# Performance work log

Measured on AMD Instinct MI355X. Metric: run time of the kernel, lower is better.

The kernel has to match this reference:

```python
import jax, jax.numpy as jnp
import numpy as np

D_MODEL = 1024
NUM_HEADS = 16
D_K = D_MODEL // NUM_HEADS  # 64
THETA = 10000.0
BATCH = 2
SEQ = 2048


def _rope_tables(positions, d_k, theta):
    # freq_k = theta**(-2k/d_k), each repeated twice (interleaved layout)
    k = jnp.arange(d_k // 2, dtype=jnp.float32)
    freq = theta ** (-2.0 * k / d_k)            # [d_k/2]
    freq = jnp.repeat(freq, 2)                  # [d_k], pattern f0,f0,f1,f1,...
    ang = positions.astype(jnp.float32)[:, None] * freq[None, :]  # [s, d_k]
    return jnp.cos(ang), jnp.sin(ang)


def _apply_rope(x, cos, sin):
    # x: [b, h, s, d_k]; interleaved rotation: y[0::2]=-x[1::2], y[1::2]=x[0::2]
    x1 = x[..., 0::2]
    x2 = x[..., 1::2]
    y = jnp.stack([-x2, x1], axis=-1).reshape(x.shape)
    return x * cos + y * sin


def setup_inputs() -> dict:
    key = jax.random.key(0)
    kx, kq, kk, kv, ko = jax.random.split(key, 5)
    sw = (2.0 / (2 * D_MODEL)) ** 0.5
    return {
        "x": jax.random.normal(kx, (BATCH, SEQ, D_MODEL), dtype=jnp.float32),
        "WQ": jax.random.normal(kq, (D_MODEL, D_MODEL), dtype=jnp.float32) * sw,
        "WK": jax.random.normal(kk, (D_MODEL, D_MODEL), dtype=jnp.float32) * sw,
        "WV": jax.random.normal(kv, (D_MODEL, D_MODEL), dtype=jnp.float32) * sw,
        "WO": jax.random.normal(ko, (D_MODEL, D_MODEL), dtype=jnp.float32) * sw,
        "token_positions": jnp.arange(SEQ, dtype=jnp.int32),
    }


def reference(x, WQ, WK, WV, WO, token_positions):
    b, s, d_model = x.shape
    h, d_k = NUM_HEADS, D_K

    # fused QKV projection: W = cat([WQ,WK,WV], 0); QKV = x @ W.T
    W = jnp.concatenate([WQ, WK, WV], axis=0)          # [3*d_model, d_model]
    QKV = jnp.einsum('bsd,ed->bse', x, W)              # [b, s, 3*d_model]
    Q, K, V = jnp.split(QKV, 3, axis=-1)               # each [b, s, d_model]

    def to_heads(t):
        return t.reshape(b, s, h, d_k).transpose(0, 2, 1, 3)  # [b, h, s, d_k]

    Q, K, V = to_heads(Q), to_heads(K), to_heads(V)

    cos, sin = _rope_tables(token_positions, d_k, THETA)       # [s, d_k]
    Q = _apply_rope(Q, cos, sin)
    K = _apply_rope(K, cos, sin)

    scale = 1.0 / jnp.sqrt(jnp.float32(d_k))
    scores = jnp.einsum('bhqd,bhkd->bhqk', Q, K) * scale       # [b,h,s,s]
    causal = jnp.tril(jnp.ones((s, s), dtype=bool))
    scores = jnp.where(causal[None, None], scores, -jnp.inf)
    probs = jax.nn.softmax(scores, axis=-1)
    attn = jnp.einsum('bhqk,bhkd->bhqd', probs, V)             # [b,h,s,d_k]
    attn = attn.transpose(0, 2, 1, 3).reshape(b, s, h * d_k)   # [b,s,d_model]
    return jnp.einsum('bsd,ed->bse', attn, WO)                 # [b,s,d_model]
```

## Files before the change

kernel.cpp:

```cpp
#include <hip/hip_runtime.h>
#include <hip/hip_bf16.h>
#include <math.h>

#define BATCH 2
#define SEQ 2048
#define DMODEL 1024
#define NHEADS 16
#define DK 64
#define BH (BATCH*NHEADS)
#define GK 1024

#define SCALE2 0.18033688011112042f
#define SHIFT  16.0f

typedef __bf16 bf16_t;
typedef __bf16 bf16x8 __attribute__((ext_vector_type(8)));
typedef __bf16 bf16x4 __attribute__((ext_vector_type(4)));
typedef float  floatx4 __attribute__((ext_vector_type(4)));

__device__ __forceinline__ void load_lds16(const bf16_t* g, bf16_t* l) {
    __builtin_amdgcn_global_load_lds(
        (const __attribute__((address_space(1))) void*)g,
        (__attribute__((address_space(3))) void*)l,
        16, 0, 0);
}

__global__ __launch_bounds__(256) void rope_tables_kernel(
    const int* __restrict__ pos, float2* __restrict__ csT)
{
    int idx = blockIdx.x * 256 + threadIdx.x;
    int kk = idx & 31, s = idx >> 5;
    float freq = exp2f((float)kk * (-13.287712379549449f / 32.0f));
    float ang = (float)pos[s] * freq;
    float sn, cs;
    sincosf(ang, &sn, &cs);
    csT[idx] = make_float2(cs, sn);
}

__global__ __launch_bounds__(256) void convert_all_kernel(
    const float* __restrict__ x,
    const float* __restrict__ WQ, const float* __restrict__ WK,
    const float* __restrict__ WV, const float* __restrict__ WO,
    bf16_t* __restrict__ xb, bf16_t* __restrict__ Wb)
{
    const int blk = blockIdx.x;
    const float* src;
    bf16_t* dst;
    int base;
    if (blk < 2048) {
        src = x; dst = xb; base = blk * 2048;
    } else {
        int wi  = (blk - 2048) >> 9;
        base = ((blk - 2048) & 511) * 2048;
        src = (wi == 0) ? WQ : (wi == 1) ? WK : (wi == 2) ? WV : WO;
        dst = Wb + (size_t)wi * DMODEL * DMODEL;
    }
    int i = base + threadIdx.x * 8;
    float4 a = *(const float4*)(src + i);
    float4 b = *(const float4*)(src + i + 4);
    bf16x8 o;
    o[0] = (bf16_t)a.x; o[1] = (bf16_t)a.y; o[2] = (bf16_t)a.z; o[3] = (bf16_t)a.w;
    o[4] = (bf16_t)b.x; o[5] = (bf16_t)b.y; o[6] = (bf16_t)b.z; o[7] = (bf16_t)b.w;
    *(bf16x8*)(dst + i) = o;
}

__device__ __forceinline__ void gemm128_mainloop(
    const bf16_t* __restrict__ Arows, const bf16_t* __restrict__ Brows,
    bf16_t (*As)[32], bf16_t (*Bs)[32], int tid, floatx4 acc[4][4])
{
    const int lane = tid & 63;
    const int w = tid >> 6;
    const int wm = w >> 1, wn = w & 1;
    const int r = lane & 15, q = lane >> 4;

    const int row0 = tid >> 2,         kc0 = (tid & 3) << 3;
    const int row1 = (tid + 256) >> 2, kc1 = kc0;

    for (int kt = 0; kt < GK; kt += 32) {
        __syncthreads();
        load_lds16(Arows + (size_t)row0 * GK + kt + kc0, &As[row0][kc0]);
        load_lds16(Arows + (size_t)row1 * GK + kt + kc1, &As[row1][kc1]);
        load_lds16(Brows + (size_t)row0 * GK + kt + kc0, &Bs[row0][kc0]);
        load_lds16(Brows + (size_t)row1 * GK + kt + kc1, &Bs[row1][kc1]);
        __syncthreads();

        bf16x8 af[4], bfr[4];
        #pragma unroll
        for (int i = 0; i < 4; ++i)
            af[i] = *(const bf16x8*)&As[wm * 64 + i * 16 + r][q << 3];
        #pragma unroll
        for (int j = 0; j < 4; ++j)
            bfr[j] = *(const bf16x8*)&Bs[wn * 64 + j * 16 + r][q << 3];

        #pragma unroll
        for (int i = 0; i < 4; ++i)
            #pragma unroll
            for (int j = 0; j < 4; ++j)
                acc[i][j] = __builtin_amdgcn_mfma_f32_16x16x32_bf16(
                    af[i], bfr[j], acc[i][j], 0, 0, 0);
    }
}

__global__ __launch_bounds__(256) void qkv_gemm_kernel(
    const bf16_t* __restrict__ x, const bf16_t* __restrict__ Wb,
    const float2* __restrict__ csT,
    bf16_t* __restrict__ Qh, bf16_t* __restrict__ Kh, bf16_t* __restrict__ Vt)
{
    __shared__ __align__(16) char qsmem[128 * 136 * 2];
    bf16_t (*As)[32]  = (bf16_t(*)[32])qsmem;
    bf16_t (*Bs)[32]  = (bf16_t(*)[32])(qsmem + 8192);
    bf16_t (*Tt)[136] = (bf16_t(*)[136])qsmem;

    const int tid = threadIdx.x;
    const int m0 = blockIdx.y * 128;
    const int n0g = blockIdx.x * 128;
    const int which = n0g >> 10;
    const int nl0 = n0g & 1023;
    const bf16_t* Wsel = Wb + (size_t)which * DMODEL * DMODEL;

    floatx4 acc[4][4];
    #pragma unroll
    for (int i = 0; i < 4; ++i)
        #pragma unroll
        for (int j = 0; j < 4; ++j)
            acc[i][j] = (floatx4){0.f, 0.f, 0.f, 0.f};

    gemm128_mainloop(x + (size_t)m0 * GK, Wsel + (size_t)nl0 * GK, As, Bs, tid, acc);
    __syncthreads();

    const int w = tid >> 6, lane = tid & 63;
    const int wm = w >> 1, wn = w & 1;
    const int r = lane & 15, qd = lane >> 4;

    if (which < 2) {
        #pragma unroll
        for (int i = 0; i < 4; ++i)
            #pragma unroll
            for (int j = 0; j < 4; ++j)
                #pragma unroll
                for (int reg = 0; reg < 4; ++reg)
                    Tt[wm * 64 + i * 16 + qd * 4 + reg][wn * 64 + j * 16 + r] =
                        (bf16_t)acc[i][j][reg];
        __syncthreads();

        bf16_t* dst = (which == 0) ? Qh : Kh;
        #pragma unroll
        for (int k2 = 0; k2 < 8; ++k2) {
            int id = tid + 256 * k2;
            int rowm = id >> 4;
            int ch = id & 15;
            int m = m0 + rowm, b = m >> 11, s = m & 2047;
            int n = nl0 + ch * 8, h = n >> 6, dk = n & 63;
            bf16x8 v = *(const bf16x8*)&Tt[rowm][ch * 8];
            const float4* csp = (const float4*)&csT[(s << 5) + (dk >> 1)];
            float4 c01 = csp[0], c23 = csp[1];
            bf16x8 o;
            float e, od;
            e = (float)v[0]; od = (float)v[1];
            o[0] = (bf16_t)(e * c01.x - od * c01.y); o[1] = (bf16_t)(od * c01.x + e * c01.y);
            e = (float)v[2]; od = (float)v[3];
            o[2] = (bf16_t)(e * c01.z - od * c01.w); o[3] = (bf16_t)(od * c01.z + e * c01.w);
            e = (float)v[4]; od = (float)v[5];
            o[4] = (bf16_t)(e * c23.x - od * c23.y); o[5] = (bf16_t)(od * c23.x + e * c23.y);
            e = (float)v[6]; od = (float)v[7];
            o[6] = (bf16_t)(e * c23.z - od * c23.w); o[7] = (bf16_t)(od * c23.z + e * c23.w);
            *(bf16x8*)(dst + (((size_t)(b << 4) + h) * SEQ + s) * DK + dk) = o;
        }
    } else {
        #pragma unroll
        for (int i = 0; i < 4; ++i)
            #pragma unroll
            for (int j = 0; j < 4; ++j) {
                int n_local = wn * 64 + j * 16 + r;
                int m_base  = wm * 64 + i * 16 + qd * 4;
                bf16x4 t;
                #pragma unroll
                for (int reg = 0; reg < 4; ++reg) t[reg] = (bf16_t)acc[i][j][reg];
                *(bf16x4*)&Tt[n_local][m_base] = t;
            }
        __syncthreads();
        const int b = m0 >> 11, s0 = m0 & 2047;
        #pragma unroll
        for (int k2 = 0; k2 < 8; ++k2) {
            int id = tid + 256 * k2;
            int row = id >> 4;
            int ch  = id & 15;
            int n = nl0 + row, h = n >> 6, dk = n & 63;
            bf16x8 val = *(const bf16x8*)&Tt[row][ch * 8];
            *(bf16x8*)(Vt + (((size_t)(b << 4) + h) * DK + dk) * SEQ + s0 + ch * 8) = val;
        }
    }
}

__global__ __launch_bounds__(512, 4) void attn_mfma_kernel(
    const bf16_t* __restrict__ Qh, const bf16_t* __restrict__ Kh,
    const bf16_t* __restrict__ Vtg, bf16_t* __restrict__ attnO)
{
    __shared__ __align__(16) char smem[55296];
    bf16_t (*Ks)[64][72] = (bf16_t(*)[64][72])smem;
    bf16_t (*Vs)[64][72] = (bf16_t(*)[64][72])(smem + 18432);
    bf16_t (*ps)[16][72] = (bf16_t(*)[16][72])(smem + 36864);
    float  (*Om)[64][68] = (float(*)[64][68])smem;
    float  (*lsum)[64]   = (float(*)[64])(smem + 36864);

    const int tid = threadIdx.x, w = tid >> 6, lane = tid & 63;
    const int grp = w >> 2, wv = w & 3;
    const int r = lane & 15, qd = lane >> 4;
    const int bh = blockIdx.y;
    const int t = tid & 255;
    const int row0 = t >> 3, c80 = (t & 7) * 8;

    const bf16_t* Kbh = Kh  + (size_t)bh * SEQ * DK;
    const bf16_t* Vbh = Vtg + (size_t)bh * DK * SEQ;
    const int b = bh >> 4, h = bh & 15;

    for (int half = 0; half < 2; ++half) {
        const int qt = half ? (int)blockIdx.x : (31 - (int)blockIdx.x);
        const int q0 = qt * 64;
        const int nIter = (qt >> 1) + 1;

        const bf16_t* Qbase = Qh + (((size_t)bh * SEQ) + q0 + wv * 16 + r) * DK;
        bf16x8 aq0 = *(const bf16x8*)(Qbase + qd * 8);
        bf16x8 aq1 = *(const bf16x8*)(Qbase + 32 + qd * 8);

        int j0 = grp * 64;
        bf16x8 pk0 = *(const bf16x8*)(Kbh + (size_t)(j0 + row0) * DK + c80);
        bf16x8 pk1 = *(const bf16x8*)(Kbh + (size_t)(j0 + row0 + 32) * DK + c80);
        bf16x8 pv0 = *(const bf16x8*)(Vbh + (size_t)row0 * SEQ + j0 + c80);
        bf16x8 pv1 = *(const bf16x8*)(Vbh + (size_t)(row0 + 32) * SEQ + j0 + c80);

        floatx4 Oa[4];
        #pragma unroll
        for (int nd = 0; nd < 4; ++nd) Oa[nd] = (floatx4){0.f, 0.f, 0.f, 0.f};
        float l_lane[4] = {0.f, 0.f, 0.f, 0.f};

        for (int it = 0; it < nIter; ++it) {
            const int kb = 2 * it + grp;
            const bool active = (kb <= qt);
            __syncthreads();
            if (active) {
                *(bf16x8*)&Ks[grp][row0][c80]      = pk0;
                *(bf16x8*)&Ks[grp][row0 + 32][c80] = pk1;
                *(bf16x8*)&Vs[grp][row0][c80]      = pv0;
                *(bf16x8*)&Vs[grp][row0 + 32][c80] = pv1;
            }
            if (kb + 2 <= qt) {
                const int j0n = (kb + 2) * 64;
                pk0 = *(const bf16x8*)(Kbh + (size_t)(j0n + row0) * DK + c80);
                pk1 = *(const bf16x8*)(Kbh + (size_t)(j0n + row0 + 32) * DK + c80);
                pv0 = *(const bf16x8*)(Vbh + (size_t)row0 * SEQ + j0n + c80);
                pv1 = *(const bf16x8*)(Vbh + (size_t)(row0 + 32) * SEQ + j0n + c80);
            }
            __syncthreads();
            if (!active) continue;

            floatx4 acc[4];
            #pragma unroll
            for (int nt = 0; nt < 4; ++nt) {
                bf16x8 bk0 = *(const bf16x8*)&Ks[grp][nt * 16 + r][qd * 8];
                bf16x8 bk1 = *(const bf16x8*)&Ks[grp][nt * 16 + r][32 + qd * 8];
                floatx4 a = (floatx4){0.f, 0.f, 0.f, 0.f};
                a = __builtin_amdgcn_mfma_f32_16x16x32_bf16(aq0, bk0, a, 0, 0, 0);
                a = __builtin_amdgcn_mfma_f32_16x16x32_bf16(aq1, bk1, a, 0, 0, 0);
                acc[nt] = a;
            }

            const bool lastb = (kb == qt);
            #pragma unroll
            for (int nt = 0; nt < 4; ++nt)
                #pragma unroll
                for (int rg = 0; rg < 4; ++rg) {
                    float s2 = fmaf(acc[nt][rg], SCALE2, -SHIFT);
                    if (lastb && (nt * 16 + r > wv * 16 + qd * 4 + rg)) s2 = -200.0f;
                    float p = exp2f(s2);
                    acc[nt][rg] = p;
                    l_lane[rg] += p;
                }

            #pragma unroll
            for (int nt = 0; nt < 4; ++nt)
                #pragma unroll
                for (int rg = 0; rg < 4; ++rg)
                    ps[w][qd * 4 + rg][nt * 16 + r] = (bf16_t)acc[nt][rg];
            bf16x8 ap0 = *(const bf16x8*)&ps[w][r][qd * 8];
            bf16x8 ap1 = *(const bf16x8*)&ps[w][r][32 + qd * 8];

            #pragma unroll
            for (int nd = 0; nd < 4; ++nd) {
                bf16x8 bv0 = *(const bf16x8*)&Vs[grp][nd * 16 + r][qd * 8];
                bf16x8 bv1 = *(const bf16x8*)&Vs[grp][nd * 16 + r][32 + qd * 8];
                floatx4 c = Oa[nd];
                c = __builtin_amdgcn_mfma_f32_16x16x32_bf16(ap0, bv0, c, 0, 0, 0);
                c = __builtin_amdgcn_mfma_f32_16x16x32_bf16(ap1, bv1, c, 0, 0, 0);
                Oa[nd] = c;
            }
        }

        __syncthreads();
        #pragma unroll
        for (int rg = 0; rg < 4; ++rg) {
            float l = l_lane[rg];
            #pragma unroll
            for (int off = 1; off < 16; off <<= 1) l += __shfl_xor(l, off);
            int rowq = wv * 16 + qd * 4 + rg;
            if (r == 0) lsum[grp][rowq] = l;
            #pragma unroll
            for (int nd = 0; nd < 4; ++nd)
                Om[grp][rowq][nd * 16 + r] = Oa[nd][rg];
        }
        __syncthreads();
        {
            int rowq = tid >> 3, c8 = (tid & 7) * 8;
            float inv = 1.0f / (lsum[0][rowq] + lsum[1][rowq]);
            float4 a0 = *(const float4*)&Om[0][rowq][c8];
            float4 a1 = *(const float4*)&Om[0][rowq][c8 + 4];
            float4 b0 = *(const float4*)&Om[1][rowq][c8];
            float4 b1 = *(const float4*)&Om[1][rowq][c8 + 4];
            bf16x8 o;
            o[0] = (bf16_t)((a0.x + b0.x) * inv);
            o[1] = (bf16_t)((a0.y + b0.y) * inv);
            o[2] = (bf16_t)((a0.z + b0.z) * inv);
            o[3] = (bf16_t)((a0.w + b0.w) * inv);
            o[4] = (bf16_t)((a1.x + b1.x) * inv);
            o[5] = (bf16_t)((a1.y + b1.y) * inv);
            o[6] = (bf16_t)((a1.z + b1.z) * inv);
            o[7] = (bf16_t)((a1.w + b1.w) * inv);
            int s = q0 + rowq;
            *(bf16x8*)(attnO + ((size_t)b * SEQ + s) * DMODEL + (h << 6) + c8) = o;
        }
    }
}

__global__ __launch_bounds__(256) void out_gemm_kernel(
    const bf16_t* __restrict__ attnI, const bf16_t* __restrict__ WOb,
    float* __restrict__ out)
{
    __shared__ __align__(16) bf16_t As[64][32];
    __shared__ __align__(16) bf16_t Bs[128][32];

    const int tid = threadIdx.x;
    const int m0 = blockIdx.y * 64;
    const int n0 = blockIdx.x * 128;
    const int lane = tid & 63, w = tid >> 6;
    const int wm = w >> 1, wn = w & 1;
    const int r = lane & 15, q = lane >> 4;

    const bf16_t* Arows = attnI + (size_t)m0 * GK;
    const bf16_t* Brows = WOb + (size_t)n0 * GK;
    const int rowA = tid >> 2, kc = (tid & 3) << 3;
    const int rowB1 = (tid + 256) >> 2;

    floatx4 acc[2][4];
    #pragma unroll
    for (int i = 0; i < 2; ++i)
        #pragma unroll
        for (int j = 0; j < 4; ++j)
            acc[i][j] = (floatx4){0.f, 0.f, 0.f, 0.f};

    for (int kt = 0; kt < GK; kt += 32) {
        __syncthreads();
        load_lds16(Arows + (size_t)rowA * GK + kt + kc, &As[rowA][kc]);
        load_lds16(Brows + (size_t)rowA * GK + kt + kc, &Bs[rowA][kc]);
        load_lds16(Brows + (size_t)rowB1 * GK + kt + kc, &Bs[rowB1][kc]);
        __syncthreads();

        bf16x8 af[2], bfr[4];
        #pragma unroll
        for (int i = 0; i < 2; ++i)
            af[i] = *(const bf16x8*)&As[wm * 32 + i * 16 + r][q << 3];
        #pragma unroll
        for (int j = 0; j < 4; ++j)
            bfr[j] = *(const bf16x8*)&Bs[wn * 64 + j * 16 + r][q << 3];

        #pragma unroll
        for (int i = 0; i < 2; ++i)
            #pragma unroll
            for (int j = 0; j < 4; ++j)
                acc[i][j] = __builtin_amdgcn_mfma_f32_16x16x32_bf16(
                    af[i], bfr[j], acc[i][j], 0, 0, 0);
    }

    #pragma unroll
    for (int i = 0; i < 2; ++i)
        #pragma unroll
        for (int j = 0; j < 4; ++j)
            #pragma unroll
            for (int reg = 0; reg < 4; ++reg) {
                int m = m0 + wm * 32 + i * 16 + q * 4 + reg;
                int n = n0 + wn * 64 + j * 16 + r;
                out[(size_t)m * DMODEL + n] = acc[i][j][reg];
            }
}

extern "C" void kernel_launch(void* const* d_in, const int* in_sizes, int n_in,
                              void* d_out, int out_size, void* d_ws, size_t ws_size,
                              hipStream_t stream)
{
    (void)in_sizes; (void)n_in; (void)out_size; (void)ws_size;

    const float* x  = (const float*)d_in[0];
    const float* WQ = (const float*)d_in[1];
    const float* WK = (const float*)d_in[2];
    const float* WV = (const float*)d_in[3];
    const float* WO = (const float*)d_in[4];
    const int* tpos = (const int*)d_in[5];
    float* out = (float*)d_out;

    bf16_t* xb   = (bf16_t*)d_ws;
    bf16_t* Wb   = xb + (size_t)BATCH * SEQ * DMODEL;
    bf16_t* Qh   = Wb + (size_t)4 * DMODEL * DMODEL;
    bf16_t* Kh   = Qh + (size_t)BH * SEQ * DK;
    bf16_t* Vt   = Kh + (size_t)BH * SEQ * DK;
    bf16_t* attn = Vt + (size_t)BH * SEQ * DK;
    float2* csT  = (float2*)(attn + (size_t)BATCH * SEQ * DMODEL);

    rope_tables_kernel<<<dim3(SEQ * 32 / 256), dim3(256), 0, stream>>>(tpos, csT);

    convert_all_kernel<<<dim3(4096), dim3(256), 0, stream>>>(
        x, WQ, WK, WV, WO, xb, Wb);

    qkv_gemm_kernel<<<dim3(3 * DMODEL / 128, BATCH * SEQ / 128), dim3(256), 0, stream>>>(
        xb, Wb, csT, Qh, Kh, Vt);

    attn_mfma_kernel<<<dim3(16, 32), dim3(512), 0, stream>>>(Qh, Kh, Vt, attn);

    out_gemm_kernel<<<dim3(DMODEL / 128, BATCH * SEQ / 64), dim3(256), 0, stream>>>(
        attn, Wb + (size_t)3 * DMODEL * DMODEL, out);
}
```

Measured before the change: 182.4 us.

## Rework attention kernel: swizzled LDS, prescaled Q, MFMA row sums, one tile per block

The softmax scale is folded into Q during the QKV epilogue, and the shift is folded into the MFMA accumulator initial value, which removes the per-element FMA. K/V/P shared-memory tiles use an XOR swizzle instead of padding, which removes bank conflicts and shrinks LDS. The S matrix is computed transposed so P can be written as packed bf16x4, and row sums come from an MFMA against a ones vector instead of shuffles. The kernel now launches one query tile per block (2x blocks) instead of pairing tiles for load balance, and sets s_setprio around the compute. Risks are load imbalance from dropping the paired scheduling and extra rounding from quantizing the prescaled Q to bf16.

```diff
diff --git a/kernel.cpp b/kernel.cpp
--- a/kernel.cpp
+++ b/kernel.cpp
@@ -144,6 +144,7 @@
         __syncthreads();
 
         bf16_t* dst = (which == 0) ? Qh : Kh;
+        const float qsc = (which == 0) ? SCALE2 : 1.0f;
         #pragma unroll
         for (int k2 = 0; k2 < 8; ++k2) {
             int id = tid + 256 * k2;
@@ -156,13 +157,13 @@
             float4 c01 = csp[0], c23 = csp[1];
             bf16x8 o;
             float e, od;
-            e = (float)v[0]; od = (float)v[1];
+            e = (float)v[0] * qsc; od = (float)v[1] * qsc;
             o[0] = (bf16_t)(e * c01.x - od * c01.y); o[1] = (bf16_t)(od * c01.x + e * c01.y);
-            e = (float)v[2]; od = (float)v[3];
+            e = (float)v[2] * qsc; od = (float)v[3] * qsc;
             o[2] = (bf16_t)(e * c01.z - od * c01.w); o[3] = (bf16_t)(od * c01.z + e * c01.w);
-            e = (float)v[4]; od = (float)v[5];
+            e = (float)v[4] * qsc; od = (float)v[5] * qsc;
             o[4] = (bf16_t)(e * c23.x - od * c23.y); o[5] = (bf16_t)(od * c23.x + e * c23.y);
-            e = (float)v[6]; od = (float)v[7];
+            e = (float)v[6] * qsc; od = (float)v[7] * qsc;
             o[6] = (bf16_t)(e * c23.z - od * c23.w); o[7] = (bf16_t)(od * c23.z + e * c23.w);
             *(bf16x8*)(dst + (((size_t)(b << 4) + h) * SEQ + s) * DK + dk) = o;
         }
@@ -196,12 +197,12 @@
     const bf16_t* __restrict__ Qh, const bf16_t* __restrict__ Kh,
     const bf16_t* __restrict__ Vtg, bf16_t* __restrict__ attnO)
 {
-    __shared__ __align__(16) char smem[55296];
-    bf16_t (*Ks)[64][72] = (bf16_t(*)[64][72])smem;
-    bf16_t (*Vs)[64][72] = (bf16_t(*)[64][72])(smem + 18432);
-    bf16_t (*ps)[16][72] = (bf16_t(*)[16][72])(smem + 36864);
-    float  (*Om)[64][68] = (float(*)[64][68])smem;
-    float  (*lsum)[64]   = (float(*)[64])(smem + 36864);
+    __shared__ __align__(16) char smem[49152];
+    bf16x8 (*Ks)[64][8]   = (bf16x8(*)[64][8])smem;
+    bf16x8 (*Vs)[64][8]   = (bf16x8(*)[64][8])(smem + 16384);
+    bf16x4 (*ps4)[16][16] = (bf16x4(*)[16][16])(smem + 32768);
+    float  (*Om)[64][68]  = (float(*)[64][68])smem;
+    float  (*lsum)[64]    = (float(*)[64])(smem + 34816);
 
     const int tid = threadIdx.x, w = tid >> 6, lane = tid & 63;
     const int grp = w >> 2, wv = w & 3;
@@ -210,124 +211,138 @@
     const int t = tid & 255;
     const int row0 = t >> 3, c80 = (t & 7) * 8;
 
+    const int R  = r & 7;
+    const int R2 = R << 1;
+    const int csw = (t & 7) ^ (row0 & 7);
+
     const bf16_t* Kbh = Kh  + (size_t)bh * SEQ * DK;
     const bf16_t* Vbh = Vtg + (size_t)bh * DK * SEQ;
     const int b = bh >> 4, h = bh & 15;
 
-    for (int half = 0; half < 2; ++half) {
-        const int qt = half ? (int)blockIdx.x : (31 - (int)blockIdx.x);
-        const int q0 = qt * 64;
-        const int nIter = (qt >> 1) + 1;
-
-        const bf16_t* Qbase = Qh + (((size_t)bh * SEQ) + q0 + wv * 16 + r) * DK;
-        bf16x8 aq0 = *(const bf16x8*)(Qbase + qd * 8);
-        bf16x8 aq1 = *(const bf16x8*)(Qbase + 32 + qd * 8);
-
-        int j0 = grp * 64;
-        bf16x8 pk0 = *(const bf16x8*)(Kbh + (size_t)(j0 + row0) * DK + c80);
-        bf16x8 pk1 = *(const bf16x8*)(Kbh + (size_t)(j0 + row0 + 32) * DK + c80);
-        bf16x8 pv0 = *(const bf16x8*)(Vbh + (size_t)row0 * SEQ + j0 + c80);
-        bf16x8 pv1 = *(const bf16x8*)(Vbh + (size_t)(row0 + 32) * SEQ + j0 + c80);
-
-        floatx4 Oa[4];
-        #pragma unroll
-        for (int nd = 0; nd < 4; ++nd) Oa[nd] = (floatx4){0.f, 0.f, 0.f, 0.f};
-        float l_lane[4] = {0.f, 0.f, 0.f, 0.f};
-
-        for (int it = 0; it < nIter; ++it) {
-            const int kb = 2 * it + grp;
-            const bool active = (kb <= qt);
-            __syncthreads();
-            if (active) {
-                *(bf16x8*)&Ks[grp][row0][c80]      = pk0;
-                *(bf16x8*)&Ks[grp][row0 + 32][c80] = pk1;
-                *(bf16x8*)&Vs[grp][row0][c80]      = pv0;
-                *(bf16x8*)&Vs[grp][row0 + 32][c80] = pv1;
-            }
-            if (kb + 2 <= qt) {
-                const int j0n = (kb + 2) * 64;
-                pk0 = *(const bf16x8*)(Kbh + (size_t)(j0n + row0) * DK + c80);
-                pk1 = *(const bf16x8*)(Kbh + (size_t)(j0n + row0 + 32) * DK + c80);
-                pv0 = *(const bf16x8*)(Vbh + (size_t)row0 * SEQ + j0n + c80);
-                pv1 = *(const bf16x8*)(Vbh + (size_t)(row0 + 32) * SEQ + j0n + c80);
-            }
-            __syncthreads();
-            if (!active) continue;
-
-            floatx4 acc[4];
-            #pragma unroll
-            for (int nt = 0; nt < 4; ++nt) {
-                bf16x8 bk0 = *(const bf16x8*)&Ks[grp][nt * 16 + r][qd * 8];
-                bf16x8 bk1 = *(const bf16x8*)&Ks[grp][nt * 16 + r][32 + qd * 8];
-                floatx4 a = (floatx4){0.f, 0.f, 0.f, 0.f};
-                a = __builtin_amdgcn_mfma_f32_16x16x32_bf16(aq0, bk0, a, 0, 0, 0);
-                a = __builtin_amdgcn_mfma_f32_16x16x32_bf16(aq1, bk1, a, 0, 0, 0);
-                acc[nt] = a;
-            }
-
-            const bool lastb = (kb == qt);
-            #pragma unroll
-            for (int nt = 0; nt < 4; ++nt)
-                #pragma unroll
-                for (int rg = 0; rg < 4; ++rg) {
-                    float s2 = fmaf(acc[nt][rg], SCALE2, -SHIFT);
-                    if (lastb && (nt * 16 + r > wv * 16 + qd * 4 + rg)) s2 = -200.0f;
-                    float p = exp2f(s2);
-                    acc[nt][rg] = p;
-                    l_lane[rg] += p;
-                }
-
+    const int qt = 31 - (int)blockIdx.x;
+    const int q0 = qt * 64;
+    const int nIter = (qt >> 1) + 1;
+
+    const bf16_t* Qbase = Qh + (((size_t)bh * SEQ) + q0 + wv * 16 + r) * DK;
+    bf16x8 aq0 = *(const bf16x8*)(Qbase + qd * 8);
+    bf16x8 aq1 = *(const bf16x8*)(Qbase + 32 + qd * 8);
+
+    bf16x8 ones;
+    #pragma unroll
+    for (int i = 0; i < 8; ++i) ones[i] = (bf16_t)1.0f;
+
+    int j0 = grp * 64;
+    bf16x8 pk0 = *(const bf16x8*)(Kbh + (size_t)(j0 + row0) * DK + c80);
+    bf16x8 pk1 = *(const bf16x8*)(Kbh + (size_t)(j0 + row0 + 32) * DK + c80);
+    bf16x8 pv0 = *(const bf16x8*)(Vbh + (size_t)row0 * SEQ + j0 + c80);
+    bf16x8 pv1 = *(const bf16x8*)(Vbh + (size_t)(row0 + 32) * SEQ + j0 + c80);
+
+    floatx4 Oa[4];
+    #pragma unroll
+    for (int nd = 0; nd < 4; ++nd) Oa[nd] = (floatx4){0.f, 0.f, 0.f, 0.f};
+    floatx4 acc_l = (floatx4){0.f, 0.f, 0.f, 0.f};
+
+    for (int it = 0; it < nIter; ++it) {
+        const int kb = 2 * it + grp;
+        const bool active = (kb <= qt);
+        __syncthreads();
+        if (active) {
+            Ks[grp][row0][csw]      = pk0;
+            Ks[grp][row0 + 32][csw] = pk1;
+            Vs[grp][row0][csw]      = pv0;
+            Vs[grp][row0 + 32][csw] = pv1;
+        }
+        if (kb + 2 <= qt) {
+            const int j0n = (kb + 2) * 64;
+            pk0 = *(const bf16x8*)(Kbh + (size_t)(j0n + row0) * DK + c80);
+            pk1 = *(const bf16x8*)(Kbh + (size_t)(j0n + row0 + 32) * DK + c80);
+            pv0 = *(const bf16x8*)(Vbh + (size_t)row0 * SEQ + j0n + c80);
+            pv1 = *(const bf16x8*)(Vbh + (size_t)(row0 + 32) * SEQ + j0n + c80);
+        }
+        __syncthreads();
+        if (!active) continue;
+
+        __builtin_amdgcn_s_setprio(1);
+        floatx4 acc[4];
+        #pragma unroll
+        for (int nt = 0; nt < 4; ++nt) {
+            bf16x8 bk0 = Ks[grp][nt * 16 + r][qd ^ R];
+            bf16x8 bk1 = Ks[grp][nt * 16 + r][(4 + qd) ^ R];
+            floatx4 a = (floatx4){-SHIFT, -SHIFT, -SHIFT, -SHIFT};
+            a = __builtin_amdgcn_mfma_f32_16x16x32_bf16(bk0, aq0, a, 0, 0, 0);
+            a = __builtin_amdgcn_mfma_f32_16x16x32_bf16(bk1, aq1, a, 0, 0, 0);
+            acc[nt] = a;
+        }
+
+        if (kb == qt) {
             #pragma unroll
             for (int nt = 0; nt < 4; ++nt)
                 #pragma unroll
                 for (int rg = 0; rg < 4; ++rg)
-                    ps[w][qd * 4 + rg][nt * 16 + r] = (bf16_t)acc[nt][rg];
-            bf16x8 ap0 = *(const bf16x8*)&ps[w][r][qd * 8];
-            bf16x8 ap1 = *(const bf16x8*)&ps[w][r][32 + qd * 8];
-
-            #pragma unroll
-            for (int nd = 0; nd < 4; ++nd) {
-                bf16x8 bv0 = *(const bf16x8*)&Vs[grp][nd * 16 + r][qd * 8];
-                bf16x8 bv1 = *(const bf16x8*)&Vs[grp][nd * 16 + r][32 + qd * 8];
-                floatx4 c = Oa[nd];
-                c = __builtin_amdgcn_mfma_f32_16x16x32_bf16(ap0, bv0, c, 0, 0, 0);
-                c = __builtin_amdgcn_mfma_f32_16x16x32_bf16(ap1, bv1, c, 0, 0, 0);
-                Oa[nd] = c;
-            }
-        }
-
-        __syncthreads();
-        #pragma unroll
-        for (int rg = 0; rg < 4; ++rg) {
-            float l = l_lane[rg];
-            #pragma unroll
-            for (int off = 1; off < 16; off <<= 1) l += __shfl_xor(l, off);
-            int rowq = wv * 16 + qd * 4 + rg;
-            if (r == 0) lsum[grp][rowq] = l;
-            #pragma unroll
-            for (int nd = 0; nd < 4; ++nd)
-                Om[grp][rowq][nd * 16 + r] = Oa[nd][rg];
-        }
-        __syncthreads();
-        {
-            int rowq = tid >> 3, c8 = (tid & 7) * 8;
-            float inv = 1.0f / (lsum[0][rowq] + lsum[1][rowq]);
-            float4 a0 = *(const float4*)&Om[0][rowq][c8];
-            float4 a1 = *(const float4*)&Om[0][rowq][c8 + 4];
-            float4 b0 = *(const float4*)&Om[1][rowq][c8];
-            float4 b1 = *(const float4*)&Om[1][rowq][c8 + 4];
-            bf16x8 o;
-            o[0] = (bf16_t)((a0.x + b0.x) * inv);
-            o[1] = (bf16_t)((a0.y + b0.y) * inv);
-            o[2] = (bf16_t)((a0.z + b0.z) * inv);
-            o[3] = (bf16_t)((a0.w + b0.w) * inv);
-            o[4] = (bf16_t)((a1.x + b1.x) * inv);
-            o[5] = (bf16_t)((a1.y + b1.y) * inv);
-            o[6] = (bf16_t)((a1.z + b1.z) * inv);
-            o[7] = (bf16_t)((a1.w + b1.w) * inv);
-            int s = q0 + rowq;
-            *(bf16x8*)(attnO + ((size_t)b * SEQ + s) * DMODEL + (h << 6) + c8) = o;
-        }
+                    if (nt * 16 + qd * 4 + rg > wv * 16 + r) acc[nt][rg] = -200.0f;
+        }
+
+        #pragma unroll
+        for (int nt = 0; nt < 4; ++nt) {
+            bf16x4 pkq;
+            #pragma unroll
+            for (int rg = 0; rg < 4; ++rg)
+                pkq[rg] = (bf16_t)exp2f(acc[nt][rg]);
+            ps4[w][r][(nt * 4 + qd) ^ R2] = pkq;
+        }
+        asm volatile("" ::: "memory");
+        __builtin_amdgcn_sched_barrier(0);
+
+        const int c0 = (qd * 2) ^ R2;
+        const int c1 = (8 + qd * 2) ^ R2;
+        bf16x4 p00 = ps4[w][r][c0], p01 = ps4[w][r][c0 + 1];
+        bf16x4 p10 = ps4[w][r][c1], p11 = ps4[w][r][c1 + 1];
+        bf16x8 ap0 = __builtin_shufflevector(p00, p01, 0, 1, 2, 3, 4, 5, 6, 7);
+        bf16x8 ap1 = __builtin_shufflevector(p10, p11, 0, 1, 2, 3, 4, 5, 6, 7);
+
+        acc_l = __builtin_amdgcn_mfma_f32_16x16x32_bf16(ap0, ones, acc_l, 0, 0, 0);
+        acc_l = __builtin_amdgcn_mfma_f32_16x16x32_bf16(ap1, ones, acc_l, 0, 0, 0);
+
+        #pragma unroll
+        for (int nd = 0; nd < 4; ++nd) {
+            bf16x8 bv0 = Vs[grp][nd * 16 + r][qd ^ R];
+            bf16x8 bv1 = Vs[grp][nd * 16 + r][(4 + qd) ^ R];
+            floatx4 c = Oa[nd];
+            c = __builtin_amdgcn_mfma_f32_16x16x32_bf16(ap0, bv0, c, 0, 0, 0);
+            c = __builtin_amdgcn_mfma_f32_16x16x32_bf16(ap1, bv1, c, 0, 0, 0);
+            Oa[nd] = c;
+        }
+        __builtin_amdgcn_s_setprio(0);
+    }
+
+    __syncthreads();
+    #pragma unroll
+    for (int rg = 0; rg < 4; ++rg) {
+        int rowq = wv * 16 + qd * 4 + rg;
+        if (r == 0) lsum[grp][rowq] = acc_l[rg];
+        #pragma unroll
+        for (int nd = 0; nd < 4; ++nd)
+            Om[grp][rowq][nd * 16 + r] = Oa[nd][rg];
+    }
+    __syncthreads();
+    {
+        int rowq = tid >> 3, c8 = (tid & 7) * 8;
+        float inv = 1.0f / (lsum[0][rowq] + lsum[1][rowq]);
+        float4 a0 = *(const float4*)&Om[0][rowq][c8];
+        float4 a1 = *(const float4*)&Om[0][rowq][c8 + 4];
+        float4 b0 = *(const float4*)&Om[1][rowq][c8];
+        float4 b1 = *(const float4*)&Om[1][rowq][c8 + 4];
+        bf16x8 o;
+        o[0] = (bf16_t)((a0.x + b0.x) * inv);
+        o[1] = (bf16_t)((a0.y + b0.y) * inv);
+        o[2] = (bf16_t)((a0.z + b0.z) * inv);
+        o[3] = (bf16_t)((a0.w + b0.w) * inv);
+        o[4] = (bf16_t)((a1.x + b1.x) * inv);
+        o[5] = (bf16_t)((a1.y + b1.y) * inv);
+        o[6] = (bf16_t)((a1.z + b1.z) * inv);
+        o[7] = (bf16_t)((a1.w + b1.w) * inv);
+        int s = q0 + rowq;
+        *(bf16x8*)(attnO + ((size_t)b * SEQ + s) * DMODEL + (h << 6) + c8) = o;
     }
 }
 
@@ -422,7 +437,7 @@
     qkv_gemm_kernel<<<dim3(3 * DMODEL / 128, BATCH * SEQ / 128), dim3(256), 0, stream>>>(
         xb, Wb, csT, Qh, Kh, Vt);
 
-    attn_mfma_kernel<<<dim3(16, 32), dim3(512), 0, stream>>>(Qh, Kh, Vt, attn);
+    attn_mfma_kernel<<<dim3(32, 32), dim3(512), 0, stream>>>(Qh, Kh, Vt, attn);
 
     out_gemm_kernel<<<dim3(DMODEL / 128, BATCH * SEQ / 64), dim3(256), 0, stream>>>(
         attn, Wb + (size_t)3 * DMODEL * DMODEL, out);
```

New measurement: 196.4 us. +7.7%, slower.
